# Kernel tuning notes

Measured on AMD Instinct MI355X. Metric: run time of the kernel, lower is better.

## Reference

```python
import jax, jax.numpy as jnp
import numpy as np

H = 12          # num_heads
T = 8           # num_temp_tokens (frames per video clip)


def _conv1d(z, w, b):
    # z: (Bv, C, T), w: (C_out, C_in, 3), padding=1, stride=1 (matches nn.Conv1d)
    y = jax.lax.conv_general_dilated(z, w, window_strides=(1,), padding=[(1, 1)],
                                     dimension_numbers=('NCH', 'OIH', 'NCH'))
    return y + b[None, :, None]


def setup_inputs() -> dict:
    key = jax.random.key(0)
    ks = jax.random.split(key, 9)
    B, N, C = 64, 197, 768
    s = 0.02
    return {
        'x': jax.random.normal(ks[0], (B, N, C), jnp.float32),
        'w_qkv': jax.random.normal(ks[1], (3 * C, C), jnp.float32) * s,
        'b_qkv': jax.random.normal(ks[2], (3 * C,), jnp.float32) * s,
        'w_proj': jax.random.normal(ks[3], (C, C), jnp.float32) * s,
        'b_proj': jax.random.normal(ks[4], (C,), jnp.float32) * s,
        'conv_q_w': jax.random.normal(ks[5], (C, C, 3), jnp.float32) * s,
        'conv_q_b': jax.random.normal(ks[6], (C,), jnp.float32) * s,
        'conv_k_w': jax.random.normal(ks[7], (C, C, 3), jnp.float32) * s,
        'conv_k_b': jax.random.normal(ks[8], (C,), jnp.float32) * s,
    }


def reference(x, w_qkv, b_qkv, w_proj, b_proj, conv_q_w, conv_q_b, conv_k_w, conv_k_b):
    B, N, C = x.shape
    Dh = C // H
    scale = Dh ** -0.5

    # temporal context from the CLS token across frames of each clip
    g = x[:, 0, :].reshape(B // T, T, C).transpose(0, 2, 1)          # (Bv, C, T)
    tcq = _conv1d(g, conv_q_w, conv_q_b).transpose(0, 2, 1).reshape(B, H, 1, Dh)
    tck = _conv1d(g, conv_k_w, conv_k_b).transpose(0, 2, 1).reshape(B, H, 1, Dh)

    qkv = (x @ w_qkv.T + b_qkv).reshape(B, N, 3, H, Dh).transpose(2, 0, 3, 1, 4)
    q, k, v = qkv[0], qkv[1], qkv[2]                                  # (B, H, N, Dh)

    # bias-added attention: (q + tcq) (k + tck)^T
    scores = jnp.einsum('bhnd,bhmd->bhnm', q + tcq, k + tck) * scale  # (B, H, N, N)
    attn = jax.nn.softmax(scores, axis=-1)
    out = jnp.einsum('bhnm,bhmd->bhnd', attn, v)                      # (B, H, N, Dh)
    out = out.transpose(0, 2, 1, 3).reshape(B, N, C)
    return out @ w_proj.T + b_proj
```

## Files before the change

kernel.cpp:

```cpp
#include <hip/hip_runtime.h>
#include <hip/hip_bf16.h>
#include <stdint.h>

typedef __attribute__((ext_vector_type(8))) short s16x8;
typedef __attribute__((ext_vector_type(4))) float f32x4;

#define MFMA16(a, b, c) __builtin_amdgcn_mfma_f32_16x16x32_bf16((a), (b), (c), 0, 0, 0)
#define SBAR() __builtin_amdgcn_s_barrier()

__device__ __forceinline__ void gl_lds16(const void* g, void* l) {
  __builtin_amdgcn_global_load_lds(
      (__attribute__((address_space(1))) void*)(void*)g,
      (__attribute__((address_space(3))) void*)l,
      16, 0, 0);
}

__device__ __forceinline__ unsigned short f2bf(float f) {
  union { float f; uint32_t u; } c; c.f = f;
  return (unsigned short)((c.u + 0x7FFFu + ((c.u >> 16) & 1u)) >> 16);
}

__device__ __forceinline__ f32x4 max4(f32x4 a, f32x4 b) {
  f32x4 c;
  c[0] = fmaxf(a[0], b[0]); c[1] = fmaxf(a[1], b[1]);
  c[2] = fmaxf(a[2], b[2]); c[3] = fmaxf(a[3], b[3]);
  return c;
}

__device__ __forceinline__ void xcd_swz(int GX, int GY, int& bx, int& by) {
  int nwg = GX * GY;
  int lid = by * GX + bx;
  int q = nwg >> 3, rm = nwg & 7;
  int xcd = lid & 7, off = lid >> 3;
  int nid = (xcd < rm ? xcd * (q + 1) : rm * (q + 1) + (xcd - rm) * q) + off;
  bx = nid % GX;
  by = nid / GX;
}

__global__ __launch_bounds__(256) void cvt_conv(
    const float* __restrict__ x, unsigned short* __restrict__ x_bf, int na4,
    const float* __restrict__ wqkv, unsigned short* __restrict__ wqkv_bf, int nb4,
    const float* __restrict__ wproj, unsigned short* __restrict__ wproj_bf, int nc4,
    const float* __restrict__ cqw, const float* __restrict__ ckw,
    float* __restrict__ tcpq, float* __restrict__ tcpk,
    const float* __restrict__ bqkv, const float* __restrict__ cqb,
    const float* __restrict__ ckb, float* __restrict__ bias_comb, int last_bid) {
  const int tid = threadIdx.x;
  const int bid = blockIdx.x;
  if (bid < 768) {
    __shared__ float g[192][10];
    const int clip = bid / 96;
    const int rem = bid % 96;
    const int chunk = rem >> 2;
    const int part = rem & 3;
    const int ci0 = part * 192;
    for (int i = tid; i < 192 * 8; i += 256) {
      int tt = i / 192, ci = i % 192;
      g[ci][tt + 1] = x[(size_t)(clip * 8 + tt) * 151296 + ci0 + ci];
    }
    for (int i = tid; i < 192; i += 256) { g[i][0] = 0.f; g[i][9] = 0.f; }
    __syncthreads();
    const int co = chunk * 32 + (tid >> 3);
    const int t = tid & 7;
    float aq = 0.f, ak = 0.f;
    const float* wqp = cqw + (size_t)co * 2304 + ci0 * 3;
    const float* wkp = ckw + (size_t)co * 2304 + ci0 * 3;
    for (int ci = 0; ci < 192; ++ci) {
      float g0 = g[ci][t], g1 = g[ci][t + 1], g2 = g[ci][t + 2];
      aq += g0 * wqp[ci * 3 + 0] + g1 * wqp[ci * 3 + 1] + g2 * wqp[ci * 3 + 2];
      ak += g0 * wkp[ci * 3 + 0] + g1 * wkp[ci * 3 + 1] + g2 * wkp[ci * 3 + 2];
    }
    int b = clip * 8 + t;
    tcpq[part * 49152 + b * 768 + co] = aq;
    tcpk[part * 49152 + b * 768 + co] = ak;
    return;
  }
  if (bid == last_bid) {
    for (int i = tid; i < 2304; i += 256) {
      float v = bqkv[i];
      if (i < 768) v += cqb[i];
      else if (i < 1536) v += ckb[i - 768];
      bias_comb[i] = v;
    }
    return;
  }
  int i = (bid - 768) * 256 + tid;
  const float* src; unsigned short* dst; int j;
  if (i < na4) { src = x; dst = x_bf; j = i; }
  else if (i < na4 + nb4) { src = wqkv; dst = wqkv_bf; j = i - na4; }
  else if (i < na4 + nb4 + nc4) { src = wproj; dst = wproj_bf; j = i - na4 - nb4; }
  else return;
  float4 v = ((const float4*)src)[j];
  ushort4 o;
  o.x = f2bf(v.x); o.y = f2bf(v.y); o.z = f2bf(v.z); o.w = f2bf(v.w);
  ((ushort4*)dst)[j] = o;
}

__global__ __launch_bounds__(1024, 4) void qkv_attn(
    const unsigned short* __restrict__ X,
    const unsigned short* __restrict__ Wq,
    const float* __restrict__ bias,
    const float* __restrict__ tcpq, const float* __restrict__ tcpk,
    unsigned short* __restrict__ O) {
  union __align__(16) Smem {
    struct {
      unsigned short Xs[3][208][64];
      unsigned short Ws[3][192][64];
    } st;
    struct {
      unsigned short Qs[208][72];
      unsigned short Ks[208][72];
      unsigned short VTs[64][232];
      unsigned short Ps[13][16][40];
    } at;
  };
  __shared__ Smem U;
  __shared__ float tcb[3][64];

  const int tid = threadIdx.x;
  const int w = tid >> 6, lane = tid & 63;
  int bx = blockIdx.x, by0 = 0;
  xcd_swz(gridDim.x, 1, bx, by0);
  const int b = bx / 12, h = bx % 12;

  if (tid < 192) {
    int sec = tid >> 6, d = tid & 63;
    float v = bias[sec * 768 + h * 64 + d];
    if (sec < 2) {
      const float* tp = (sec == 0) ? tcpq : tcpk;
      int idx = b * 768 + h * 64 + d;
#pragma unroll
      for (int p = 0; p < 4; ++p) v += tp[p * 49152 + idx];
    }
    tcb[sec][d] = v;
  }

  const int wm = w >> 2, wn = w & 3;
  const int r = lane & 15, gq = lane >> 4;
  const int lrow = lane >> 3;
  const int lsw = ((lane & 7) ^ (lrow & 7)) * 8;
  const int mfn = (wm == 3) ? 4 : 3;

  f32x4 acc[4][3] = {};
  const size_t xbase = (size_t)b * 197 * 768;

  const int swzk[2] = { ((0 + gq) ^ (r & 7)) * 16, ((4 + gq) ^ (r & 7)) * 16 };
  const int rowA = (wm * 48 + r) * 128;
  const int rowB = (wn * 48 + r) * 128;

  auto stage = [&](int buf, int kc) {
#pragma unroll
    for (int j = 0; j < 2; ++j) {
      int c = w + j * 16;
      if (c < 26) {
        int row = c * 8 + lrow;
        gl_lds16(X + xbase + (size_t)row * 768 + kc * 64 + lsw,
                 (char*)&U.st.Xs[buf][0][0] + c * 1024);
      }
    }
#pragma unroll
    for (int j = 0; j < 2; ++j) {
      int c = w + j * 16;
      if (c < 24) {
        int wrow = c * 8 + lrow;
        int sec = wrow >> 6;
        gl_lds16(Wq + (size_t)(sec * 768 + h * 64 + (wrow & 63)) * 768 + kc * 64 + lsw,
                 (char*)&U.st.Ws[buf][0][0] + c * 1024);
      }
    }
  };

#define WAIT_OWN()                                                 \
  do {                                                             \
    if (w < 8)       asm volatile("s_waitcnt vmcnt(4)" ::: "memory"); \
    else if (w < 10) asm volatile("s_waitcnt vmcnt(3)" ::: "memory"); \
    else             asm volatile("s_waitcnt vmcnt(2)" ::: "memory"); \
  } while (0)

  stage(0, 0);
  stage(1, 1);
  WAIT_OWN();
  SBAR();

#pragma unroll
  for (int kc = 0; kc < 12; ++kc) {
    if (kc + 2 < 12) stage((kc + 2) % 3, kc + 2);
    const char* xb = (const char*)&U.st.Xs[kc % 3][0][0] + rowA;
    const char* wb = (const char*)&U.st.Ws[kc % 3][0][0] + rowB;
    __builtin_amdgcn_s_setprio(1);
#pragma unroll
    for (int kk = 0; kk < 2; ++kk) {
      s16x8 bfrg[3];
#pragma unroll
      for (int nf = 0; nf < 3; ++nf)
        bfrg[nf] = *(const s16x8*)(wb + nf * 2048 + swzk[kk]);
#pragma unroll
      for (int mf = 0; mf < 4; ++mf) {
        if (mf < mfn) {
          s16x8 afr = *(const s16x8*)(xb + mf * 2048 + swzk[kk]);
#pragma unroll
          for (int nf = 0; nf < 3; ++nf) acc[mf][nf] = MFMA16(afr, bfrg[nf], acc[mf][nf]);
        }
      }
    }
    __builtin_amdgcn_s_setprio(0);
    if (kc < 10) {
      WAIT_OWN();
      SBAR();
    } else if (kc == 10) {
      asm volatile("s_waitcnt vmcnt(0)" ::: "memory");
      SBAR();
    }
  }
  __syncthreads();

  for (int i = tid; i < 64 * 35; i += 1024) {
    int d = i / 35, c = 197 + i % 35;
    U.at.VTs[d][c] = 0;
  }
#pragma unroll
  for (int mf = 0; mf < 4; ++mf) {
    if (mf < mfn) {
#pragma unroll
      for (int nf = 0; nf < 3; ++nf) {
        int ncol = wn * 48 + nf * 16 + r;
        int sec = ncol >> 6, d = ncol & 63;
        float bb = tcb[sec][d];
#pragma unroll
        for (int rr = 0; rr < 4; ++rr) {
          int mrow = wm * 48 + mf * 16 + gq * 4 + rr;
          unsigned short bv = f2bf(acc[mf][nf][rr] + bb);
          if (sec == 0)      U.at.Qs[mrow][d] = bv;
          else if (sec == 1) U.at.Ks[mrow][d] = bv;
          else if (mrow < 197) U.at.VTs[d][mrow] = bv;
        }
      }
    }
  }
  __syncthreads();

  const int g = gq;
  for (int qt = w; qt < 13; qt += 16) {
    const int q0 = qt * 16;
    int qrow = q0 + r; if (qrow > 196) qrow = 196;
    s16x8 aq0 = *(const s16x8*)&U.at.Qs[qrow][g * 8];
    s16x8 aq1 = *(const s16x8*)&U.at.Qs[qrow][32 + g * 8];

    f32x4 s[13];
    __builtin_amdgcn_s_setprio(1);
#pragma unroll
    for (int j = 0; j < 13; ++j) {
      f32x4 z = {};
      z = MFMA16(aq0, *(const s16x8*)&U.at.Ks[j * 16 + r][g * 8], z);
      z = MFMA16(aq1, *(const s16x8*)&U.at.Ks[j * 16 + r][32 + g * 8], z);
      s[j] = z;
    }
    __builtin_amdgcn_s_setprio(0);
    if (r >= 5) { s[12][0] = -1e30f; s[12][1] = -1e30f; s[12][2] = -1e30f; s[12][3] = -1e30f; }

    f32x4 mx = s[0];
#pragma unroll
    for (int j = 1; j < 13; ++j) mx = max4(mx, s[j]);
#pragma unroll
    for (int off = 1; off < 16; off <<= 1) {
      f32x4 o_;
      o_[0] = __shfl_xor(mx[0], off, 64); o_[1] = __shfl_xor(mx[1], off, 64);
      o_[2] = __shfl_xor(mx[2], off, 64); o_[3] = __shfl_xor(mx[3], off, 64);
      mx = max4(mx, o_);
    }
    const float cexp = 0.125f * 1.44269504088896f;
    f32x4 sum = {};
#pragma unroll
    for (int j = 0; j < 13; ++j) {
      f32x4 p;
      p[0] = exp2f((s[j][0] - mx[0]) * cexp); p[1] = exp2f((s[j][1] - mx[1]) * cexp);
      p[2] = exp2f((s[j][2] - mx[2]) * cexp); p[3] = exp2f((s[j][3] - mx[3]) * cexp);
      s[j] = p;
      sum += p;
    }
#pragma unroll
    for (int off = 1; off < 16; off <<= 1) {
      sum[0] += __shfl_xor(sum[0], off, 64); sum[1] += __shfl_xor(sum[1], off, 64);
      sum[2] += __shfl_xor(sum[2], off, 64); sum[3] += __shfl_xor(sum[3], off, 64);
    }

    f32x4 o4[4] = {};
    for (int ks = 0; ks < 7; ++ks) {
      int j0 = ks * 2;
#pragma unroll
      for (int jj = 0; jj < 2; ++jj) {
        int jt = j0 + jj;
        int colb = jj * 16 + r;
        if (jt < 13) {
          f32x4 p = s[jt < 13 ? jt : 0];
          U.at.Ps[w][g * 4 + 0][colb] = f2bf(p[0]);
          U.at.Ps[w][g * 4 + 1][colb] = f2bf(p[1]);
          U.at.Ps[w][g * 4 + 2][colb] = f2bf(p[2]);
          U.at.Ps[w][g * 4 + 3][colb] = f2bf(p[3]);
        } else {
          U.at.Ps[w][g * 4 + 0][colb] = 0; U.at.Ps[w][g * 4 + 1][colb] = 0;
          U.at.Ps[w][g * 4 + 2][colb] = 0; U.at.Ps[w][g * 4 + 3][colb] = 0;
        }
      }
      asm volatile("s_waitcnt lgkmcnt(0)" ::: "memory");
      s16x8 ap = *(const s16x8*)&U.at.Ps[w][r][g * 8];
      __builtin_amdgcn_s_setprio(1);
#pragma unroll
      for (int n = 0; n < 4; ++n)
        o4[n] = MFMA16(ap, *(const s16x8*)&U.at.VTs[n * 16 + r][ks * 32 + g * 8], o4[n]);
      __builtin_amdgcn_s_setprio(0);
    }

    f32x4 rinv;
    rinv[0] = 1.0f / sum[0]; rinv[1] = 1.0f / sum[1];
    rinv[2] = 1.0f / sum[2]; rinv[3] = 1.0f / sum[3];
#pragma unroll
    for (int n = 0; n < 4; ++n) {
#pragma unroll
      for (int rr = 0; rr < 4; ++rr) {
        int qr = q0 + g * 4 + rr;
        if (qr < 197)
          O[((size_t)(b * 197 + qr)) * 768 + h * 64 + n * 16 + r] = f2bf(o4[n][rr] * rinv[rr]);
      }
    }
  }
#undef WAIT_OWN
}

__global__ __launch_bounds__(1024, 4) void proj_gemm(
    const unsigned short* __restrict__ A,
    const unsigned short* __restrict__ Bw,
    const float* __restrict__ bias,
    float* __restrict__ Out) {
  __shared__ __align__(16) unsigned short Xs[3][208][64];
  __shared__ __align__(16) unsigned short Ws[3][192][64];
  const int tid = threadIdx.x;
  const int w = tid >> 6, lane = tid & 63;
  int bx = blockIdx.x, by0 = 0;
  xcd_swz(gridDim.x, 1, bx, by0);
  const int b = bx >> 2, nt = bx & 3;
  const int wm = w >> 2, wn = w & 3;
  const int r = lane & 15, gq = lane >> 4;
  const int lrow = lane >> 3;
  const int lsw = ((lane & 7) ^ (lrow & 7)) * 8;
  const int mfn = (wm == 3) ? 4 : 3;

  f32x4 acc[4][3] = {};
  const size_t abase = (size_t)b * 197 * 768;
  const int swzk[2] = { ((0 + gq) ^ (r & 7)) * 16, ((4 + gq) ^ (r & 7)) * 16 };
  const int rowA = (wm * 48 + r) * 128;
  const int rowB = (wn * 48 + r) * 128;

  auto stage = [&](int buf, int kc) {
#pragma unroll
    for (int j = 0; j < 2; ++j) {
      int c = w + j * 16;
      if (c < 26) {
        int row = c * 8 + lrow;
        gl_lds16(A + abase + (size_t)row * 768 + kc * 64 + lsw,
                 (char*)&Xs[buf][0][0] + c * 1024);
      }
    }
#pragma unroll
    for (int j = 0; j < 2; ++j) {
      int c = w + j * 16;
      if (c < 24) {
        int wrow = c * 8 + lrow;
        gl_lds16(Bw + (size_t)(nt * 192 + wrow) * 768 + kc * 64 + lsw,
                 (char*)&Ws[buf][0][0] + c * 1024);
      }
    }
  };

#define WAIT_OWN()                                                 \
  do {                                                             \
    if (w < 8)       asm volatile("s_waitcnt vmcnt(4)" ::: "memory"); \
    else if (w < 10) asm volatile("s_waitcnt vmcnt(3)" ::: "memory"); \
    else             asm volatile("s_waitcnt vmcnt(2)" ::: "memory"); \
  } while (0)

  stage(0, 0);
  stage(1, 1);
  WAIT_OWN();
  SBAR();

#pragma unroll
  for (int kc = 0; kc < 12; ++kc) {
    if (kc + 2 < 12) stage((kc + 2) % 3, kc + 2);
    const char* xb = (const char*)&Xs[kc % 3][0][0] + rowA;
    const char* wb = (const char*)&Ws[kc % 3][0][0] + rowB;
    __builtin_amdgcn_s_setprio(1);
#pragma unroll
    for (int kk = 0; kk < 2; ++kk) {
      s16x8 bfrg[3];
#pragma unroll
      for (int nf = 0; nf < 3; ++nf)
        bfrg[nf] = *(const s16x8*)(wb + nf * 2048 + swzk[kk]);
#pragma unroll
      for (int mf = 0; mf < 4; ++mf) {
        if (mf < mfn) {
          s16x8 afr = *(const s16x8*)(xb + mf * 2048 + swzk[kk]);
#pragma unroll
          for (int nf = 0; nf < 3; ++nf) acc[mf][nf] = MFMA16(afr, bfrg[nf], acc[mf][nf]);
        }
      }
    }
    __builtin_amdgcn_s_setprio(0);
    if (kc < 10) {
      WAIT_OWN();
      SBAR();
    } else if (kc == 10) {
      asm volatile("s_waitcnt vmcnt(0)" ::: "memory");
      SBAR();
    }
  }

#pragma unroll
  for (int mf = 0; mf < 4; ++mf) {
    if (mf < mfn) {
#pragma unroll
      for (int nf = 0; nf < 3; ++nf) {
        int N = nt * 192 + wn * 48 + nf * 16 + r;
        float bb = bias[N];
#pragma unroll
        for (int rr = 0; rr < 4; ++rr) {
          int mrow = wm * 48 + mf * 16 + gq * 4 + rr;
          if (mrow < 197)
            Out[((size_t)(b * 197 + mrow)) * 768 + N] = acc[mf][nf][rr] + bb;
        }
      }
    }
  }
#undef WAIT_OWN
}

extern "C" void kernel_launch(void* const* d_in, const int* in_sizes, int n_in,
                              void* d_out, int out_size, void* d_ws, size_t ws_size,
                              hipStream_t stream) {
  const float* x       = (const float*)d_in[0];
  const float* w_qkv   = (const float*)d_in[1];
  const float* b_qkv   = (const float*)d_in[2];
  const float* w_proj  = (const float*)d_in[3];
  const float* b_proj  = (const float*)d_in[4];
  const float* conv_qw = (const float*)d_in[5];
  const float* conv_qb = (const float*)d_in[6];
  const float* conv_kw = (const float*)d_in[7];
  const float* conv_kb = (const float*)d_in[8];
  float* out = (float*)d_out;

  char* ws = (char*)d_ws;
  size_t off = 0;
  auto alloc = [&](size_t n) {
    char* p = ws + off;
    off = (off + n + 255) & ~(size_t)255;
    return p;
  };
  unsigned short* x_bf    = (unsigned short*)alloc(12608ull * 768 * 2);
  unsigned short* ao_bf   = (unsigned short*)alloc(12608ull * 768 * 2);
  unsigned short* wqkv_bf = (unsigned short*)alloc(2304ull * 768 * 2);
  unsigned short* wproj_bf= (unsigned short*)alloc(768ull * 768 * 2);
  float* tcpq = (float*)alloc(4ull * 64 * 768 * 4);
  float* tcpk = (float*)alloc(4ull * 64 * 768 * 4);
  float* bias_comb = (float*)alloc(2304ull * 4);
  if (off > ws_size) return;

  const int na4 = 2420736, nb4 = 442368, nc4 = 147456;
  const int cvt_blocks = (na4 + nb4 + nc4 + 255) / 256;
  const int last_bid = 768 + cvt_blocks;
  cvt_conv<<<dim3(last_bid + 1), 256, 0, stream>>>(
      x, x_bf, na4, w_qkv, wqkv_bf, nb4, w_proj, wproj_bf, nc4,
      conv_qw, conv_kw, tcpq, tcpk,
      b_qkv, conv_qb, conv_kb, bias_comb, last_bid);
  qkv_attn<<<dim3(768), 1024, 0, stream>>>(x_bf, wqkv_bf, bias_comb, tcpq, tcpk, ao_bf);
  proj_gemm<<<dim3(256), 1024, 0, stream>>>(ao_bf, wproj_bf, b_proj, out);
}
```

Before: 150.3 us.

## Retile projection GEMM as flat 128x128 tiles with double buffering

```diff
diff --git a/kernel.cpp b/kernel.cpp
--- a/kernel.cpp
+++ b/kernel.cpp
@@ -327,111 +327,93 @@
 #undef WAIT_OWN
 }
 
-__global__ __launch_bounds__(1024, 4) void proj_gemm(
+__global__ __launch_bounds__(512, 4) void proj_gemm(
     const unsigned short* __restrict__ A,
     const unsigned short* __restrict__ Bw,
     const float* __restrict__ bias,
     float* __restrict__ Out) {
-  __shared__ __align__(16) unsigned short Xs[3][208][64];
-  __shared__ __align__(16) unsigned short Ws[3][192][64];
+  __shared__ __align__(16) unsigned short As[2][128][64];
+  __shared__ __align__(16) unsigned short Bs[2][128][64];
   const int tid = threadIdx.x;
   const int w = tid >> 6, lane = tid & 63;
-  int bx = blockIdx.x, by0 = 0;
-  xcd_swz(gridDim.x, 1, bx, by0);
-  const int b = bx >> 2, nt = bx & 3;
   const int wm = w >> 2, wn = w & 3;
   const int r = lane & 15, gq = lane >> 4;
+  int bx = blockIdx.x, by = blockIdx.y;
+  xcd_swz(gridDim.x, gridDim.y, bx, by);
+  const int m0 = by * 128, n0 = bx * 128;
   const int lrow = lane >> 3;
   const int lsw = ((lane & 7) ^ (lrow & 7)) * 8;
-  const int mfn = (wm == 3) ? 4 : 3;
-
-  f32x4 acc[4][3] = {};
-  const size_t abase = (size_t)b * 197 * 768;
   const int swzk[2] = { ((0 + gq) ^ (r & 7)) * 16, ((4 + gq) ^ (r & 7)) * 16 };
-  const int rowA = (wm * 48 + r) * 128;
-  const int rowB = (wn * 48 + r) * 128;
-
-  auto stage = [&](int buf, int kc) {
+  const int rowA = (wm * 64 + r) * 128;
+  const int rowB = (wn * 32 + r) * 128;
+
+  f32x4 acc[4][2] = {};
+
+  auto stage = [&](int buf, int kt) {
 #pragma unroll
     for (int j = 0; j < 2; ++j) {
-      int c = w + j * 16;
-      if (c < 26) {
-        int row = c * 8 + lrow;
-        gl_lds16(A + abase + (size_t)row * 768 + kc * 64 + lsw,
-                 (char*)&Xs[buf][0][0] + c * 1024);
-      }
+      int c = w + j * 8;
+      int row = c * 8 + lrow;
+      gl_lds16(A + (size_t)(m0 + row) * 768 + kt * 64 + lsw, (char*)&As[buf][0][0] + c * 1024);
     }
 #pragma unroll
     for (int j = 0; j < 2; ++j) {
-      int c = w + j * 16;
-      if (c < 24) {
-        int wrow = c * 8 + lrow;
-        gl_lds16(Bw + (size_t)(nt * 192 + wrow) * 768 + kc * 64 + lsw,
-                 (char*)&Ws[buf][0][0] + c * 1024);
-      }
+      int c = w + j * 8;
+      int row = c * 8 + lrow;
+      gl_lds16(Bw + (size_t)(n0 + row) * 768 + kt * 64 + lsw, (char*)&Bs[buf][0][0] + c * 1024);
     }
   };
-
-#define WAIT_OWN()                                                 \
-  do {                                                             \
-    if (w < 8)       asm volatile("s_waitcnt vmcnt(4)" ::: "memory"); \
-    else if (w < 10) asm volatile("s_waitcnt vmcnt(3)" ::: "memory"); \
-    else             asm volatile("s_waitcnt vmcnt(2)" ::: "memory"); \
-  } while (0)
 
   stage(0, 0);
   stage(1, 1);
-  WAIT_OWN();
+  asm volatile("s_waitcnt vmcnt(4)" ::: "memory");
   SBAR();
 
 #pragma unroll
-  for (int kc = 0; kc < 12; ++kc) {
-    if (kc + 2 < 12) stage((kc + 2) % 3, kc + 2);
-    const char* xb = (const char*)&Xs[kc % 3][0][0] + rowA;
-    const char* wb = (const char*)&Ws[kc % 3][0][0] + rowB;
+  for (int kt = 0; kt < 12; ++kt) {
+    const int cur = kt & 1;
+    const char* xb = (const char*)&As[cur][0][0] + rowA;
+    const char* wb = (const char*)&Bs[cur][0][0] + rowB;
+    s16x8 af[2][4], bfr[2][2];
+#pragma unroll
+    for (int kk = 0; kk < 2; ++kk) {
+#pragma unroll
+      for (int m = 0; m < 4; ++m) af[kk][m] = *(const s16x8*)(xb + m * 2048 + swzk[kk]);
+#pragma unroll
+      for (int n = 0; n < 2; ++n) bfr[kk][n] = *(const s16x8*)(wb + n * 2048 + swzk[kk]);
+    }
+    asm volatile("s_waitcnt lgkmcnt(0)" ::: "memory");
+    __builtin_amdgcn_sched_barrier(0);
+    SBAR();
+    if (kt + 2 < 12) stage(cur, kt + 2);
     __builtin_amdgcn_s_setprio(1);
 #pragma unroll
-    for (int kk = 0; kk < 2; ++kk) {
-      s16x8 bfrg[3];
-#pragma unroll
-      for (int nf = 0; nf < 3; ++nf)
-        bfrg[nf] = *(const s16x8*)(wb + nf * 2048 + swzk[kk]);
-#pragma unroll
-      for (int mf = 0; mf < 4; ++mf) {
-        if (mf < mfn) {
-          s16x8 afr = *(const s16x8*)(xb + mf * 2048 + swzk[kk]);
-#pragma unroll
-          for (int nf = 0; nf < 3; ++nf) acc[mf][nf] = MFMA16(afr, bfrg[nf], acc[mf][nf]);
-        }
-      }
-    }
+    for (int kk = 0; kk < 2; ++kk)
+#pragma unroll
+      for (int m = 0; m < 4; ++m)
+#pragma unroll
+        for (int n = 0; n < 2; ++n) acc[m][n] = MFMA16(af[kk][m], bfr[kk][n], acc[m][n]);
     __builtin_amdgcn_s_setprio(0);
-    if (kc < 10) {
-      WAIT_OWN();
+    if (kt < 11) {
+      if (kt < 10) asm volatile("s_waitcnt vmcnt(4)" ::: "memory");
+      else         asm volatile("s_waitcnt vmcnt(0)" ::: "memory");
       SBAR();
-    } else if (kc == 10) {
-      asm volatile("s_waitcnt vmcnt(0)" ::: "memory");
-      SBAR();
-    }
-  }
-
-#pragma unroll
-  for (int mf = 0; mf < 4; ++mf) {
-    if (mf < mfn) {
-#pragma unroll
-      for (int nf = 0; nf < 3; ++nf) {
-        int N = nt * 192 + wn * 48 + nf * 16 + r;
-        float bb = bias[N];
-#pragma unroll
-        for (int rr = 0; rr < 4; ++rr) {
-          int mrow = wm * 48 + mf * 16 + gq * 4 + rr;
-          if (mrow < 197)
-            Out[((size_t)(b * 197 + mrow)) * 768 + N] = acc[mf][nf][rr] + bb;
-        }
-      }
-    }
-  }
-#undef WAIT_OWN
+    }
+  }
+
+#pragma unroll
+  for (int m = 0; m < 4; ++m) {
+#pragma unroll
+    for (int n = 0; n < 2; ++n) {
+      int N = n0 + wn * 32 + n * 16 + r;
+      float bb = bias[N];
+#pragma unroll
+      for (int rr = 0; rr < 4; ++rr) {
+        int M = m0 + wm * 64 + m * 16 + gq * 4 + rr;
+        if (M < 12608) Out[(size_t)M * 768 + N] = acc[m][n][rr] + bb;
+      }
+    }
+  }
 }
 
 extern "C" void kernel_launch(void* const* d_in, const int* in_sizes, int n_in,
@@ -472,5 +454,5 @@
       conv_qw, conv_kw, tcpq, tcpk,
       b_qkv, conv_qb, conv_kb, bias_comb, last_bid);
   qkv_attn<<<dim3(768), 1024, 0, stream>>>(x_bf, wqkv_bf, bias_comb, tcpq, tcpk, ao_bf);
-  proj_gemm<<<dim3(256), 1024, 0, stream>>>(ao_bf, wproj_bf, b_proj, out);
-}
+  proj_gemm<<<dim3(6, 99), 512, 0, stream>>>(ao_bf, wproj_bf, b_proj, out);
+}
```

Measured after the change: 161.9 us. 7.7% more time.
